# Performance work log

Measured on AMD Instinct MI355X. Metric: run time of the kernel, lower is better.

## Reference

```python
import jax, jax.numpy as jnp
import numpy as np

BN, T, D_MODEL = 128, 256, 128
D_INNER, D_STATE, D_CONV, DT_RANK = 2 * D_MODEL, 16, 4, 8  # mamba-ssm defaults


def silu(v):
    return v * jax.nn.sigmoid(v)


def setup_inputs() -> dict:
    key = jax.random.key(0)
    ks = jax.random.split(key, 8)
    s = 0.02
    A_log = jnp.log(jnp.tile(jnp.arange(1, D_STATE + 1, dtype=jnp.float32), (D_INNER, 1)))
    return {
        "x": jax.random.normal(ks[0], (BN, T, D_MODEL), jnp.float32),
        "in_proj_w": jax.random.normal(ks[1], (2 * D_INNER, D_MODEL), jnp.float32) * s,
        "conv_w": jax.random.normal(ks[2], (D_INNER, 1, D_CONV), jnp.float32) * s,
        "conv_b": jnp.zeros((D_INNER,), jnp.float32),
        "x_proj_w": jax.random.normal(ks[3], (DT_RANK + 2 * D_STATE, D_INNER), jnp.float32) * s,
        "dt_proj_w": jax.random.normal(ks[4], (D_INNER, DT_RANK), jnp.float32) * s,
        "dt_proj_b": jax.random.uniform(ks[5], (D_INNER,), jnp.float32, -4.0, -2.0),
        "A_log": A_log,
        "D": jnp.ones((D_INNER,), jnp.float32),
        "out_proj_w": jax.random.normal(ks[6], (D_MODEL, D_INNER), jnp.float32) * s,
        "down_w": jax.random.normal(ks[7], (D_MODEL, D_MODEL, 3), jnp.float32) * s,
        "down_b": jnp.zeros((D_MODEL,), jnp.float32),
        "ln_g": jnp.ones((D_MODEL,), jnp.float32),
        "ln_b": jnp.zeros((D_MODEL,), jnp.float32),
    }


def _mamba(x, in_proj_w, conv_w, conv_b, x_proj_w, dt_proj_w, dt_proj_b, A_log, D, out_proj_w):
    B = x.shape[0]
    xz = jnp.einsum('bld,ed->ble', x, in_proj_w)            # (B,L,2*di)
    xc, z = jnp.split(xz, 2, axis=-1)
    # depthwise causal conv over time
    xt = xc.transpose(0, 2, 1)                               # (B,di,L)
    xt = jax.lax.conv_general_dilated(xt, conv_w, (1,), [(D_CONV - 1, 0)],
                                      feature_group_count=D_INNER)
    xc = silu((xt + conv_b[None, :, None]).transpose(0, 2, 1))  # (B,L,di)
    x_dbl = jnp.einsum('bld,ed->ble', xc, x_proj_w)
    dt, Bm, Cm = jnp.split(x_dbl, [DT_RANK, DT_RANK + D_STATE], axis=-1)
    delta = jax.nn.softplus(jnp.einsum('blr,dr->bld', dt, dt_proj_w) + dt_proj_b)  # (B,L,di)
    A = -jnp.exp(A_log)                                       # (di,N)

    def step(h, inp):
        d_t, B_t, C_t, u_t = inp                              # (B,di),(B,N),(B,N),(B,di)
        dA = jnp.exp(d_t[..., None] * A)                      # (B,di,N)
        h = dA * h + (d_t * u_t)[..., None] * B_t[:, None, :]
        return h, jnp.einsum('bdn,bn->bd', h, C_t)

    h0 = jnp.zeros((B, D_INNER, D_STATE), x.dtype)
    _, ys = jax.lax.scan(step, h0, (delta.swapaxes(0, 1), Bm.swapaxes(0, 1),
                                    Cm.swapaxes(0, 1), xc.swapaxes(0, 1)))
    y = ys.swapaxes(0, 1) + xc * D                            # (B,L,di)
    y = y * silu(z)
    return jnp.einsum('ble,de->bld', y, out_proj_w)


def reference(x, in_proj_w, conv_w, conv_b, x_proj_w, dt_proj_w, dt_proj_b,
              A_log, D, out_proj_w, down_w, down_b, ln_g, ln_b):
    x_skip = x
    h = _mamba(x, in_proj_w, conv_w, conv_b, x_proj_w, dt_proj_w, dt_proj_b,
               A_log, D, out_proj_w)                          # dropout: eval mode = identity
    ht = h.transpose(0, 2, 1)                                 # (B,d,T)
    ht = jax.lax.conv_general_dilated(ht, down_w, (2,), [(1, 1)]) + down_b[None, :, None]
    h = ht.transpose(0, 2, 1)                                 # (B,T//2,d)
    mu = jnp.mean(h, axis=-1, keepdims=True)
    var = jnp.mean((h - mu) ** 2, axis=-1, keepdims=True)
    h = (h - mu) * jax.lax.rsqrt(var + 1e-5) * ln_g + ln_b
    return (h, x_skip)
```

## Files before the change

### kernel.cpp

```cpp
#include <hip/hip_runtime.h>
#include <hip/hip_bf16.h>


typedef __attribute__((ext_vector_type(8))) short bf16x8;
typedef __attribute__((ext_vector_type(4))) short bf16x4;
typedef __attribute__((ext_vector_type(4))) float f32x4;
using bf16 = __hip_bfloat16;

static __device__ __forceinline__ short f2s(float v) {
  union { bf16 b; short s; } u; u.b = (bf16)v; return u.s;
}
static __device__ __forceinline__ float s2f(short s) {
  union { short s; bf16 b; } u; u.s = s; return (float)u.b;
}
static __device__ __forceinline__ bf16x8 ld8f(const float* __restrict__ p) {
  f32x4 a = *(const f32x4*)p;
  f32x4 b = *(const f32x4*)(p + 4);
  bf16x8 r;
  r[0] = f2s(a[0]); r[1] = f2s(a[1]); r[2] = f2s(a[2]); r[3] = f2s(a[3]);
  r[4] = f2s(b[0]); r[5] = f2s(b[1]); r[6] = f2s(b[2]); r[7] = f2s(b[3]);
  return r;
}

static __device__ __forceinline__ size_t pidx(int b, int d, int t) {
  return ((((size_t)b * 8 + (d >> 5)) * 32 + (t >> 3)) * 32 + (d & 31)) * 8 + (t & 7);
}

__global__ __launch_bounds__(256, 2) void front_k(const float* __restrict__ x,
                                                  const float* __restrict__ ipw,
                                                  const float* __restrict__ xpw,
                                                  const float* __restrict__ dwn,
                                                  const float* __restrict__ opw,
                                                  const float* __restrict__ cw,
                                                  const float* __restrict__ cb,
                                                  const float* __restrict__ dtw,
                                                  const float* __restrict__ dtb,
                                                  short* __restrict__ xcP,
                                                  short* __restrict__ dP,
                                                  short* __restrict__ zP,
                                                  float* __restrict__ SBC,
                                                  float* __restrict__ out1,
                                                  short* __restrict__ G) {
  const int b  = blockIdx.x >> 2;
  const int t0 = (blockIdx.x & 3) * 64;
  const int w    = threadIdx.x >> 6;
  const int lane = threadIdx.x & 63;
  const int r16  = lane & 15;
  const int quad = lane >> 4;
  __shared__ short AL[80][136];
  __shared__ short XC[80][264];
  __shared__ short LT[64][72];
  __shared__ float DTL[64][8];
  if (blockIdx.x < 384) {
    const int k  = blockIdx.x >> 7;
    const int co = blockIdx.x & 127;
    const int e  = threadIdx.x;
    float acc = 0.f;
#pragma unroll 4
    for (int dm = 0; dm < 128; ++dm) {
      acc += dwn[(co * 128 + dm) * 3 + k] * opw[dm * 256 + e];
    }
    G[(size_t)(k * 128 + co) * 256 + e] = f2s(acc);
  }
  for (int c = threadIdx.x; c < 1280; c += 256) {
    const int row = c >> 4;
    const int col = (c & 15) * 8;
    const int t = t0 - 16 + row;
    bf16x8 v = {};
    if (t >= 0) {
      const float* src = x + ((size_t)(b * 256 + t)) * 128 + col;
      f32x4 f0 = *(const f32x4*)src;
      f32x4 f1 = *(const f32x4*)(src + 4);
      v[0] = f2s(f0[0]); v[1] = f2s(f0[1]); v[2] = f2s(f0[2]); v[3] = f2s(f0[3]);
      v[4] = f2s(f1[0]); v[5] = f2s(f1[1]); v[6] = f2s(f1[2]); v[7] = f2s(f1[3]);
      if (row >= 16) {
        float* dst = out1 + ((size_t)(b * 256 + t)) * 128 + col;
        *(f32x4*)dst = f0;
        *(f32x4*)(dst + 4) = f1;
      }
    }
    *(bf16x8*)(&AL[row][col]) = v;
  }
  __syncthreads();
  {
    f32x4 acc[5][4] = {};
#pragma unroll
    for (int ks = 0; ks < 4; ++ks) {
      const int k0 = ks * 32;
      bf16x8 wf[4];
#pragma unroll
      for (int j = 0; j < 4; ++j)
        wf[j] = ld8f(ipw + (size_t)(w * 64 + j * 16 + r16) * 128 + quad * 8 + k0);
#pragma unroll
      for (int mt = 0; mt < 5; ++mt) {
        bf16x8 a = *(const bf16x8*)(&AL[mt * 16 + r16][quad * 8 + k0]);
#pragma unroll
        for (int j = 0; j < 4; ++j)
          acc[mt][j] = __builtin_amdgcn_mfma_f32_16x16x32_bf16(a, wf[j],
                                                               acc[mt][j], 0, 0, 0);
      }
    }
#pragma unroll
    for (int mt = 0; mt < 5; ++mt)
#pragma unroll
      for (int j = 0; j < 4; ++j)
#pragma unroll
        for (int r = 0; r < 4; ++r)
          XC[mt * 16 + quad * 4 + r][w * 64 + j * 16 + r16] = f2s(acc[mt][j][r]);
  }
  for (int nt = 0; nt < 4; ++nt) {
    f32x4 accz[4] = {};
#pragma unroll
    for (int ks = 0; ks < 4; ++ks) {
      const int k0 = ks * 32;
      bf16x8 a = *(const bf16x8*)(&AL[16 + w * 16 + r16][quad * 8 + k0]);
#pragma unroll
      for (int j = 0; j < 4; ++j) {
        bf16x8 wf = ld8f(ipw +
                 (size_t)(256 + nt * 64 + j * 16 + r16) * 128 + quad * 8 + k0);
        accz[j] = __builtin_amdgcn_mfma_f32_16x16x32_bf16(a, wf, accz[j], 0, 0, 0);
      }
    }
    __syncthreads();
#pragma unroll
    for (int j = 0; j < 4; ++j)
#pragma unroll
      for (int r = 0; r < 4; ++r) {
        float v = accz[j][r];
        LT[j * 16 + r16][w * 16 + quad * 4 + r] = f2s(v / (1.f + __expf(-v)));
      }
    __syncthreads();
#pragma unroll
    for (int it = 0; it < 2; ++it) {
      const int dw = (threadIdx.x >> 3) + it * 32;
      const int tc = (threadIdx.x & 7) * 8;
      bf16x8 v = *(const bf16x8*)(&LT[dw][tc]);
      *(bf16x8*)(zP + pidx(b, nt * 64 + dw, t0 + tc)) = v;
    }
  }
  __syncthreads();
  bf16x8 cv[4][2];
#pragma unroll
  for (int dt_ = 0; dt_ < 4; ++dt_) {
    const int d = dt_ * 64 + lane;
    const float w0 = cw[d * 4], w1 = cw[d * 4 + 1];
    const float w2 = cw[d * 4 + 2], w3 = cw[d * 4 + 3];
    const float bias = cb[d];
    const int rb_ = 16 + w * 16;
    float p0 = s2f(XC[rb_ - 3][d]);
    float p1 = s2f(XC[rb_ - 2][d]);
    float p2 = s2f(XC[rb_ - 1][d]);
#pragma unroll
    for (int i = 0; i < 16; ++i) {
      const float cur = s2f(XC[rb_ + i][d]);
      const float a = bias + p0 * w0 + p1 * w1 + p2 * w2 + cur * w3;
      const short s = f2s(a / (1.f + __expf(-a)));
      cv[dt_][i >> 3][i & 7] = s;
      p0 = p1; p1 = p2; p2 = cur;
    }
    *(bf16x8*)(xcP + pidx(b, d, t0 + w * 16))     = cv[dt_][0];
    *(bf16x8*)(xcP + pidx(b, d, t0 + w * 16 + 8)) = cv[dt_][1];
  }
  __syncthreads();
#pragma unroll
  for (int dt_ = 0; dt_ < 4; ++dt_) {
    const int d = dt_ * 64 + lane;
#pragma unroll
    for (int i = 0; i < 16; ++i)
      XC[16 + w * 16 + i][d] = cv[dt_][i >> 3][i & 7];
  }
  __syncthreads();
  {
    f32x4 ax[3] = {};
#pragma unroll
    for (int ks = 0; ks < 8; ++ks) {
      const int k0 = ks * 32;
      bf16x8 a = *(const bf16x8*)(&XC[16 + w * 16 + r16][quad * 8 + k0]);
#pragma unroll
      for (int j = 0; j < 3; ++j) {
        const int wr = j * 16 + r16;
        bf16x8 wf = {};
        if (wr < 40) wf = ld8f(xpw + (size_t)wr * 256 + quad * 8 + k0);
        ax[j] = __builtin_amdgcn_mfma_f32_16x16x32_bf16(a, wf, ax[j], 0, 0, 0);
      }
    }
#pragma unroll
    for (int j = 0; j < 3; ++j) {
      const int col = j * 16 + r16;
#pragma unroll
      for (int r = 0; r < 4; ++r) {
        const int tl = w * 16 + quad * 4 + r;
        if (col < 8) {
          DTL[tl][col] = ax[j][r];
        } else if (col < 40) {
          SBC[((size_t)b * 256 + t0 + tl) * 32 + (col - 8)] = ax[j][r];
        }
      }
    }
  }
  __syncthreads();
#pragma unroll
  for (int dt_ = 0; dt_ < 4; ++dt_) {
    const int d = dt_ * 64 + lane;
    float wd[8];
#pragma unroll
    for (int j = 0; j < 8; ++j) wd[j] = dtw[d * 8 + j];
    const float bd = dtb[d];
    bf16x8 dv0, dv1;
#pragma unroll
    for (int i = 0; i < 16; ++i) {
      const int tl = w * 16 + i;
      const f32x4 p0 = *(const f32x4*)(&DTL[tl][0]);
      const f32x4 p1 = *(const f32x4*)(&DTL[tl][4]);
      float acc = bd;
#pragma unroll
      for (int j = 0; j < 4; ++j) acc += p0[j] * wd[j] + p1[j] * wd[4 + j];
      const float delta = (acc > 20.f) ? acc : __logf(1.f + __expf(acc));
      const short s = f2s(delta);
      if (i < 8) dv0[i] = s; else dv1[i - 8] = s;
    }
    *(bf16x8*)(dP + pidx(b, d, t0 + w * 16))     = dv0;
    *(bf16x8*)(dP + pidx(b, d, t0 + w * 16 + 8)) = dv1;
  }
}

#define LDS_S(SB, CH) do {                                                   \
    _Pragma("unroll")                                                        \
    for (int j_ = 0; j_ < 8; ++j_) {                                         \
      SBr[SB][j_] = *(const f32x4*)(&S[(CH) * 8 + j_][q * 4]);               \
      SCr[SB][j_] = *(const f32x4*)(&S[(CH) * 8 + j_][16 + q * 4]);          \
    }                                                                        \
  } while (0)

#define LDG(GB, CH) do {                                                     \
    if ((CH) < 32) {                                                         \
      uu[GB] = *(const bf16x8*)(xcP + pb + (size_t)(CH) * 256);              \
      dd[GB] = *(const bf16x8*)(dP + pb + (size_t)(CH) * 256);               \
      if (q == 0) zz[GB] = *(const bf16x8*)(zP + pb + (size_t)(CH) * 256);   \
    }                                                                        \
  } while (0)

#define CHUNK(GB, SB, CH) do {                                               \
    _Pragma("unroll")                                                        \
    for (int tt_ = 0; tt_ < 8; ++tt_) {                                      \
      const int t_ = (CH) * 8 + tt_;                                         \
      const float delta_ = s2f(dd[GB][tt_]);                                 \
      const float u_ = s2f(uu[GB][tt_]);                                     \
      const float du_ = delta_ * u_;                                         \
      const f32x4 Bq_ = SBr[SB][tt_];                                        \
      const f32x4 Cq_ = SCr[SB][tt_];                                        \
      float yt_ = 0.f;                                                       \
      _Pragma("unroll")                                                      \
      for (int n_ = 0; n_ < 4; ++n_) {                                       \
        const float dA_ = __builtin_amdgcn_exp2f(delta_ * A2[n_]);           \
        h[n_] = dA_ * h[n_] + du_ * Bq_[n_];                                 \
        yt_ += h[n_] * Cq_[n_];                                              \
      }                                                                      \
      yt_ += __shfl_xor(yt_, 1);                                             \
      yt_ += __shfl_xor(yt_, 2);                                             \
      if (q == 0)                                                            \
        yb[(rb + t_) * 256 + d] = f2s((yt_ + u_ * Dv) * s2f(zz[GB][tt_]));   \
    }                                                                        \
  } while (0)

__global__ __launch_bounds__(128, 2) void scan12(const float* __restrict__ SBC,
                                                 const short* __restrict__ xcP,
                                                 const short* __restrict__ dP,
                                                 const short* __restrict__ zP,
                                                 const float* __restrict__ alog,
                                                 const float* __restrict__ Dp,
                                                 short* __restrict__ yb) {
  const int g = blockIdx.x & 7;
  const int b = blockIdx.x >> 3;
  const int q = threadIdx.x & 3;
  const int dl = threadIdx.x >> 2;
  const int d = g * 32 + dl;
  const size_t rb = (size_t)b * 256;
  __shared__ float S[256][32];
  for (int i = threadIdx.x; i < 2048; i += 128) {
    *(f32x4*)(&S[i >> 3][(i & 7) * 4]) =
        *(const f32x4*)(SBC + (size_t)b * 8192 + i * 4);
  }
  float A2[4];
#pragma unroll
  for (int n = 0; n < 4; ++n)
    A2[n] = -__expf(alog[d * 16 + q * 4 + n]) * 1.44269504089f;
  const float Dv = Dp[d];
  float h[4] = {0.f, 0.f, 0.f, 0.f};
  const size_t pb = (((size_t)b * 8 + g) * 32) * 256 + (size_t)dl * 8;
  f32x4 SBr[2][8], SCr[2][8];
  bf16x8 uu[4], dd[4];
  bf16x8 zz[4] = {};
  LDG(0, 0); LDG(1, 1); LDG(2, 2); LDG(3, 3);
  __syncthreads();
  LDS_S(0, 0);
  for (int c = 0; c < 32; c += 4) {
    LDS_S(1, c + 1);
    CHUNK(0, 0, c);
    LDG(0, c + 4);
    LDS_S(0, c + 2);
    CHUNK(1, 1, c + 1);
    LDG(1, c + 5);
    LDS_S(1, c + 3);
    CHUNK(2, 0, c + 2);
    LDG(2, c + 6);
    if (c + 4 < 32) LDS_S(0, c + 4);
    CHUNK(3, 1, c + 3);
    LDG(3, c + 7);
  }
}

__global__ __launch_bounds__(256) void od_k(const short* __restrict__ yb,
                                            const short* __restrict__ G,
                                            const float* __restrict__ db,
                                            const float* __restrict__ lng,
                                            const float* __restrict__ lnb,
                                            float* __restrict__ out) {
  const int wave = threadIdx.x >> 6;
  const int lane = threadIdx.x & 63;
  const int r16  = lane & 15;
  const int quad = lane >> 4;
  const int m_base = blockIdx.x * 64 + wave * 16;
  const int ma = m_base + r16;
  const int ba = ma >> 7, toa = ma & 127;
  f32x4 acc[8] = {};
  const bf16x8 az = {};
#pragma unroll
  for (int k = 0; k < 3; ++k) {
    const int tp = 2 * toa + k - 1;
    const bool valid = (tp >= 0) && (tp < 256);
    const int tpc = tp < 0 ? 0 : (tp > 255 ? 255 : tp);
    const short* Ap = yb + (size_t)(ba * 256 + tpc) * 256 + quad * 8;
    const short* Gp = G + (size_t)(k * 128 + r16) * 256 + quad * 8;
#pragma unroll
    for (int k0 = 0; k0 < 256; k0 += 32) {
      bf16x8 a = *(const bf16x8*)(Ap + k0);
      a = valid ? a : az;
#pragma unroll
      for (int j = 0; j < 8; ++j) {
        bf16x8 g = *(const bf16x8*)(Gp + (size_t)j * 16 * 256 + k0);
        acc[j] = __builtin_amdgcn_mfma_f32_16x16x32_bf16(a, g, acc[j], 0, 0, 0);
      }
    }
  }
  float dbv[8], g8[8], be8[8];
#pragma unroll
  for (int j = 0; j < 8; ++j) {
    const int col = j * 16 + r16;
    dbv[j] = db[col]; g8[j] = lng[col]; be8[j] = lnb[col];
  }
#pragma unroll
  for (int r = 0; r < 4; ++r) {
    float v[8];
    float s = 0.f;
#pragma unroll
    for (int j = 0; j < 8; ++j) { v[j] = acc[j][r] + dbv[j]; s += v[j]; }
    s += __shfl_xor(s, 1); s += __shfl_xor(s, 2);
    s += __shfl_xor(s, 4); s += __shfl_xor(s, 8);
    const float mu = s * (1.0f / 128.0f);
    float vs = 0.f;
#pragma unroll
    for (int j = 0; j < 8; ++j) { const float dd = v[j] - mu; vs += dd * dd; }
    vs += __shfl_xor(vs, 1); vs += __shfl_xor(vs, 2);
    vs += __shfl_xor(vs, 4); vs += __shfl_xor(vs, 8);
    const float rstd = rsqrtf(vs * (1.0f / 128.0f) + 1e-5f);
    const int rowm = m_base + quad * 4 + r;
#pragma unroll
    for (int j = 0; j < 8; ++j) {
      out[(size_t)rowm * 128 + j * 16 + r16] = (v[j] - mu) * rstd * g8[j] + be8[j];
    }
  }
}

static const size_t O_YB    = 0;
static const size_t O_XCP   = 16777216;
static const size_t O_ZP    = 33554432;
static const size_t O_DP    = 50331648;
static const size_t O_SBC   = 67108864;
static const size_t O_G     = 71303168;

extern "C" void kernel_launch(void* const* d_in, const int* in_sizes, int n_in,
                              void* d_out, int out_size, void* d_ws, size_t ws_size,
                              hipStream_t stream) {
  const float* x    = (const float*)d_in[0];
  const float* ipw  = (const float*)d_in[1];
  const float* cw   = (const float*)d_in[2];
  const float* cb   = (const float*)d_in[3];
  const float* xpw  = (const float*)d_in[4];
  const float* dtw  = (const float*)d_in[5];
  const float* dtb  = (const float*)d_in[6];
  const float* alog = (const float*)d_in[7];
  const float* Dp   = (const float*)d_in[8];
  const float* opw  = (const float*)d_in[9];
  const float* dw   = (const float*)d_in[10];
  const float* db   = (const float*)d_in[11];
  const float* lng  = (const float*)d_in[12];
  const float* lnb  = (const float*)d_in[13];

  char*  ws     = (char*)d_ws;
  short* yb     = (short*)(ws + O_YB);
  short* xcP    = (short*)(ws + O_XCP);
  short* zP     = (short*)(ws + O_ZP);
  short* dP     = (short*)(ws + O_DP);
  float* SBC    = (float*)(ws + O_SBC);
  short* G      = (short*)(ws + O_G);
  float* out    = (float*)d_out;
  float* out1   = out + 2097152;

  front_k<<<512, 256, 0, stream>>>(x, ipw, xpw, dw, opw, cw, cb, dtw, dtb,
                                   xcP, dP, zP, SBC, out1, G);
  scan12<<<1024, 128, 0, stream>>>(SBC, xcP, dP, zP, alog, Dp, yb);
  od_k<<<256, 256, 0, stream>>>(yb, G, db, lng, lnb, out);
}
```

Baseline: 241.6 us.

## Pre-convert projection weights to bf16 and move fused out/down weight product into scan

```diff
diff --git a/kernel.cpp b/kernel.cpp
--- a/kernel.cpp
+++ b/kernel.cpp
@@ -13,24 +13,28 @@
 static __device__ __forceinline__ float s2f(short s) {
   union { short s; bf16 b; } u; u.s = s; return (float)u.b;
 }
-static __device__ __forceinline__ bf16x8 ld8f(const float* __restrict__ p) {
-  f32x4 a = *(const f32x4*)p;
-  f32x4 b = *(const f32x4*)(p + 4);
-  bf16x8 r;
-  r[0] = f2s(a[0]); r[1] = f2s(a[1]); r[2] = f2s(a[2]); r[3] = f2s(a[3]);
-  r[4] = f2s(b[0]); r[5] = f2s(b[1]); r[6] = f2s(b[2]); r[7] = f2s(b[3]);
-  return r;
-}
 
 static __device__ __forceinline__ size_t pidx(int b, int d, int t) {
   return ((((size_t)b * 8 + (d >> 5)) * 32 + (t >> 3)) * 32 + (d & 31)) * 8 + (t & 7);
 }
 
+__global__ __launch_bounds__(256) void prep_w(const float* __restrict__ ipw,
+                                              const float* __restrict__ xpw,
+                                              short* __restrict__ ipwb,
+                                              short* __restrict__ wxb) {
+  int idx = blockIdx.x * 256 + threadIdx.x;
+  if (idx < 65536) {
+    ipwb[idx] = f2s(ipw[idx]);
+  } else {
+    int j = idx - 65536;
+    int n = j >> 8;
+    wxb[j] = (n < 40) ? f2s(xpw[j]) : (short)0;
+  }
+}
+
 __global__ __launch_bounds__(256, 2) void front_k(const float* __restrict__ x,
-                                                  const float* __restrict__ ipw,
-                                                  const float* __restrict__ xpw,
-                                                  const float* __restrict__ dwn,
-                                                  const float* __restrict__ opw,
+                                                  const short* __restrict__ ipwb,
+                                                  const short* __restrict__ wxb,
                                                   const float* __restrict__ cw,
                                                   const float* __restrict__ cb,
                                                   const float* __restrict__ dtw,
@@ -39,8 +43,7 @@
                                                   short* __restrict__ dP,
                                                   short* __restrict__ zP,
                                                   float* __restrict__ SBC,
-                                                  float* __restrict__ out1,
-                                                  short* __restrict__ G) {
+                                                  float* __restrict__ out1) {
   const int b  = blockIdx.x >> 2;
   const int t0 = (blockIdx.x & 3) * 64;
   const int w    = threadIdx.x >> 6;
@@ -51,17 +54,6 @@
   __shared__ short XC[80][264];
   __shared__ short LT[64][72];
   __shared__ float DTL[64][8];
-  if (blockIdx.x < 384) {
-    const int k  = blockIdx.x >> 7;
-    const int co = blockIdx.x & 127;
-    const int e  = threadIdx.x;
-    float acc = 0.f;
-#pragma unroll 4
-    for (int dm = 0; dm < 128; ++dm) {
-      acc += dwn[(co * 128 + dm) * 3 + k] * opw[dm * 256 + e];
-    }
-    G[(size_t)(k * 128 + co) * 256 + e] = f2s(acc);
-  }
   for (int c = threadIdx.x; c < 1280; c += 256) {
     const int row = c >> 4;
     const int col = (c & 15) * 8;
@@ -90,7 +82,8 @@
       bf16x8 wf[4];
 #pragma unroll
       for (int j = 0; j < 4; ++j)
-        wf[j] = ld8f(ipw + (size_t)(w * 64 + j * 16 + r16) * 128 + quad * 8 + k0);
+        wf[j] = *(const bf16x8*)(ipwb +
+                 (size_t)(w * 64 + j * 16 + r16) * 128 + quad * 8 + k0);
 #pragma unroll
       for (int mt = 0; mt < 5; ++mt) {
         bf16x8 a = *(const bf16x8*)(&AL[mt * 16 + r16][quad * 8 + k0]);
@@ -116,7 +109,7 @@
       bf16x8 a = *(const bf16x8*)(&AL[16 + w * 16 + r16][quad * 8 + k0]);
 #pragma unroll
       for (int j = 0; j < 4; ++j) {
-        bf16x8 wf = ld8f(ipw +
+        bf16x8 wf = *(const bf16x8*)(ipwb +
                  (size_t)(256 + nt * 64 + j * 16 + r16) * 128 + quad * 8 + k0);
         accz[j] = __builtin_amdgcn_mfma_f32_16x16x32_bf16(a, wf, accz[j], 0, 0, 0);
       }
@@ -178,9 +171,7 @@
       bf16x8 a = *(const bf16x8*)(&XC[16 + w * 16 + r16][quad * 8 + k0]);
 #pragma unroll
       for (int j = 0; j < 3; ++j) {
-        const int wr = j * 16 + r16;
-        bf16x8 wf = {};
-        if (wr < 40) wf = ld8f(xpw + (size_t)wr * 256 + quad * 8 + k0);
+        bf16x8 wf = *(const bf16x8*)(wxb + (size_t)(j * 16 + r16) * 256 + quad * 8 + k0);
         ax[j] = __builtin_amdgcn_mfma_f32_16x16x32_bf16(a, wf, ax[j], 0, 0, 0);
       }
     }
@@ -269,7 +260,24 @@
                                                  const short* __restrict__ zP,
                                                  const float* __restrict__ alog,
                                                  const float* __restrict__ Dp,
+                                                 const float* __restrict__ dwn,
+                                                 const float* __restrict__ opw,
+                                                 short* __restrict__ G,
                                                  short* __restrict__ yb) {
+  if (blockIdx.x >= 1024) {
+    const int jb  = blockIdx.x - 1024;
+    const int k   = jb >> 8;
+    const int rem = jb & 255;
+    const int co  = rem >> 1;
+    const int e   = (rem & 1) * 128 + threadIdx.x;
+    float acc = 0.f;
+#pragma unroll 4
+    for (int dm = 0; dm < 128; ++dm) {
+      acc += dwn[(co * 128 + dm) * 3 + k] * opw[dm * 256 + e];
+    }
+    G[(size_t)(k * 128 + co) * 256 + e] = f2s(acc);
+    return;
+  }
   const int g = blockIdx.x & 7;
   const int b = blockIdx.x >> 3;
   const int q = threadIdx.x & 3;
@@ -378,6 +386,7 @@
 static const size_t O_DP    = 50331648;
 static const size_t O_SBC   = 67108864;
 static const size_t O_G     = 71303168;
+static const size_t O_IPWB  = 92274688;
 
 extern "C" void kernel_launch(void* const* d_in, const int* in_sizes, int n_in,
                               void* d_out, int out_size, void* d_ws, size_t ws_size,
@@ -404,11 +413,14 @@
   short* dP     = (short*)(ws + O_DP);
   float* SBC    = (float*)(ws + O_SBC);
   short* G      = (short*)(ws + O_G);
+  short* ipwb   = (short*)(ws + O_IPWB);
   float* out    = (float*)d_out;
+  short* wxb    = (short*)out;
   float* out1   = out + 2097152;
 
-  front_k<<<512, 256, 0, stream>>>(x, ipw, xpw, dw, opw, cw, cb, dtw, dtb,
-                                   xcP, dP, zP, SBC, out1, G);
-  scan12<<<1024, 128, 0, stream>>>(SBC, xcP, dP, zP, alog, Dp, yb);
+  prep_w<<<320, 256, 0, stream>>>(ipw, xpw, ipwb, wxb);
+  front_k<<<512, 256, 0, stream>>>(x, ipwb, wxb, cw, cb, dtw, dtb,
+                                   xcP, dP, zP, SBC, out1);
+  scan12<<<1792, 128, 0, stream>>>(SBC, xcP, dP, zP, alog, Dp, dw, opw, G, yb);
   od_k<<<256, 256, 0, stream>>>(yb, G, db, lng, lnb, out);
 }
```

After: 219.2 us. 1.1x faster.
